# Kernel optimization log

Hardware: AMD Instinct MI355X
Metric: run time of the kernel (lower is better)

## Reference

```python
import jax, jax.numpy as jnp
import numpy as np

I, H, O, K = 64, 512, 3, 6  # input, hidden, output classes, num heads


def setup_inputs() -> dict:
    key = jax.random.key(0)
    ks = jax.random.split(key, 8)
    B, T = 256, 512
    s = 0.05
    return {
        "x": jax.random.normal(ks[0], (B, T, I), dtype=jnp.float32),
        "W_ih": jax.random.normal(ks[1], (4 * H, I), dtype=jnp.float32) * s,
        "W_hh": jax.random.normal(ks[2], (4 * H, H), dtype=jnp.float32) * s,
        "b_ih": jax.random.normal(ks[3], (4 * H,), dtype=jnp.float32) * s,
        "b_hh": jax.random.normal(ks[4], (4 * H,), dtype=jnp.float32) * s,
        "W_heads": jax.random.normal(ks[5], (K, O, H), dtype=jnp.float32) * s,
        "b_heads": jax.random.normal(ks[6], (K, O), dtype=jnp.float32) * s,
    }


def _lstm_last_h(x, W_ih, W_hh, b_ih, b_hh):
    # x: [B, T, I]; returns final hidden state h_T: [B, H]
    B = x.shape[0]
    h0 = jnp.zeros((B, H), dtype=x.dtype)
    c0 = jnp.zeros((B, H), dtype=x.dtype)
    # precompute input projections for all timesteps: [T, B, 4H]
    x_proj = jnp.einsum('bti,gi->tbg', x, W_ih) + b_ih + b_hh

    def step(carry, xp_t):
        h, c = carry
        gates = xp_t + h @ W_hh.T  # [B, 4H]
        i_g, f_g, g_g, o_g = jnp.split(gates, 4, axis=-1)  # PyTorch gate order i,f,g,o
        i_g = jax.nn.sigmoid(i_g)
        f_g = jax.nn.sigmoid(f_g)
        g_g = jnp.tanh(g_g)
        o_g = jax.nn.sigmoid(o_g)
        c = f_g * c + i_g * g_g
        h = o_g * jnp.tanh(c)
        return (h, c), None

    (h_T, _), _ = jax.lax.scan(step, (h0, c0), x_proj)
    return h_T


def reference(x, W_ih, W_hh, b_ih, b_hh, W_heads, b_heads):
    h_T = _lstm_last_h(x, W_ih, W_hh, b_ih, b_hh)  # [B, H]
    # six parallel linear heads on last hidden state -> stacked [6, B, O]
    out = jnp.einsum('koh,bh->kbo', W_heads, h_T) + b_heads[:, None, :]
    return out
```

## Files before the change

### kernel.cpp

```cpp
#include <hip/hip_runtime.h>
#include <hip/hip_bf16.h>
#include <cstdint>

#define TSTEPS 512
#define BATCH  256
#define HID    512
#define INP    64
#define NGRP   16
#define GROWS  16
#define NSL    16
#define NWG    256
#define KTH    16
#define RING   8

typedef __attribute__((ext_vector_type(8))) short short8;
typedef __attribute__((ext_vector_type(4))) float f32x4;
typedef __attribute__((ext_vector_type(2))) float f32x2;
typedef __attribute__((ext_vector_type(2))) unsigned long long ull2;

#define HB_OFF    0
#define HT_OFF    (RING*BATCH*HID*2)
#define FLAGS_OFF (HT_OFF + BATCH*HID*4)
#define FLAGS_SZ  (NGRP*TSTEPS*4)
#define CNT_OFF   (FLAGS_OFF + FLAGS_SZ)
#define ZERO2_SZ  (FLAGS_SZ + 64)

__device__ __forceinline__ unsigned cvtpk(float a, float b) {
    unsigned r;
    asm("v_cvt_pk_bf16_f32 %0, %1, %2" : "=v"(r) : "v"(a), "v"(b));
    return r;
}
__device__ __forceinline__ short8 pack8(float4 a0, float4 a1) {
    uint4 u = { cvtpk(a0.x, a0.y), cvtpk(a0.z, a0.w),
                cvtpk(a1.x, a1.y), cvtpk(a1.z, a1.w) };
    return __builtin_bit_cast(short8, u);
}
__device__ __forceinline__ float sigm(float x)  { return 1.0f/(1.0f + __expf(-x)); }
__device__ __forceinline__ float tanhf_(float x){ return 2.0f/(1.0f + __expf(-2.0f*x)) - 1.0f; }

__global__ void __launch_bounds__(256, 1)
lstm_persist(const float* __restrict__ x,   const float* __restrict__ Wih,
             const float* __restrict__ Whh, const float* __restrict__ bih,
             const float* __restrict__ bhh, const float* __restrict__ Whead,
             const float* __restrict__ bhead, float* __restrict__ out,
             char* __restrict__ ws)
{
    extern __shared__ char lds[];
    const int tid  = threadIdx.x;
    const int lane = tid & 63;
    const int wv   = tid >> 6;
    const int l15  = lane & 15, lq = lane >> 4, l7 = lane & 7;

    unsigned short* hb = (unsigned short*)(ws + HB_OFF);
    float* hT  = (float*)(ws + HT_OFF);
    int* flags = (int*)(ws + FLAGS_OFF);
    int* cnt   = (int*)(ws + CNT_OFF);

    int* org = (int*)(lds + 131056);
    if (tid == 0) {
        unsigned xcd;
        asm volatile("s_getreg_b32 %0, hwreg(HW_REG_XCC_ID)" : "=s"(xcd));
        xcd &= 7u;
        int slot = __hip_atomic_fetch_add(&cnt[xcd], 1, __ATOMIC_RELAXED, __HIP_MEMORY_SCOPE_AGENT) & 31;
        org[0] = (int)xcd * 2 + (slot >> 4);
        org[1] = slot & 15;
    }
    __syncthreads();
    const int g  = org[0];
    const int sl = org[1];
    const int hbase = sl*32 + wv*8;
    const int gsel  = l15 >> 3;

    short8 whh[KTH][2];
    #pragma unroll
    for (int kt = 0; kt < KTH; ++kt)
        #pragma unroll
        for (int nt = 0; nt < 2; ++nt) {
            int grow = (nt*2 + gsel)*HID + hbase + l7;
            const float4* p = (const float4*)(Whh + (size_t)grow*HID + kt*32 + lq*8);
            whh[kt][nt] = pack8(p[0], p[1]);
        }
    short8 wihf[2][2];
    #pragma unroll
    for (int kt = 0; kt < 2; ++kt)
        #pragma unroll
        for (int nt = 0; nt < 2; ++nt) {
            int grow = (nt*2 + gsel)*HID + hbase + l7;
            const float4* p = (const float4*)(Wih + (size_t)grow*INP + kt*32 + lq*8);
            wihf[kt][nt] = pack8(p[0], p[1]);
        }
    float bias0, bias1;
    { int gr = (0*2 + gsel)*HID + hbase + l7; bias0 = bih[gr] + bhh[gr]; }
    { int gr = (1*2 + gsel)*HID + hbase + l7; bias1 = bih[gr] + bhh[gr]; }

    unsigned short* hgrp = hb + (size_t)g*GROWS*HID;
    float*          hTg  = hT + (size_t)g*GROWS*HID;
    int* flg = flags + g*TSTEPS;

    const int skt = tid >> 4, sr = tid & 15;
    char* swp = lds + skt*1024 + sr*16;
    const char* srp = lds + lane*16;

    const float* xrow = x + ((size_t)(g*GROWS + l15)*TSTEPS)*INP + lq*8;

    f32x2 cst = {0.f, 0.f};
    const bool lo = (l15 < 8);

    float4 xv0 = *(const float4*)(xrow);
    float4 xv1 = *(const float4*)(xrow + 4);
    float4 xv2 = *(const float4*)(xrow + 32);
    float4 xv3 = *(const float4*)(xrow + 36);

    #pragma clang loop unroll(disable)
    for (int t = 0; t < TSTEPS; ++t) {
        f32x4 a0 = {bias0, bias0, bias0, bias0};
        f32x4 a1 = {bias1, bias1, bias1, bias1};
        f32x4 b0 = {0.f, 0.f, 0.f, 0.f};
        f32x4 b1 = {0.f, 0.f, 0.f, 0.f};
        {
            short8 af0 = pack8(xv0, xv1);
            short8 af1 = pack8(xv2, xv3);
            a0 = __builtin_amdgcn_mfma_f32_16x16x32_bf16(af0, wihf[0][0], a0, 0, 0, 0);
            a1 = __builtin_amdgcn_mfma_f32_16x16x32_bf16(af0, wihf[0][1], a1, 0, 0, 0);
            b0 = __builtin_amdgcn_mfma_f32_16x16x32_bf16(af1, wihf[1][0], b0, 0, 0, 0);
            b1 = __builtin_amdgcn_mfma_f32_16x16x32_bf16(af1, wihf[1][1], b1, 0, 0, 0);
        }
        __builtin_amdgcn_sched_barrier(0);

        if (t) {
            if (lane == 0) {
                const int* fl = flg + (t-1);
                while (__hip_atomic_load(fl, __ATOMIC_RELAXED, __HIP_MEMORY_SCOPE_AGENT) < NSL) {}
            }
            __builtin_amdgcn_sched_barrier(0);
            asm volatile("" ::: "memory");
        }

        {
            const char* gsrc = (const char*)(hgrp + (size_t)(t & (RING-1))*BATCH*HID)
                               + sr*1024 + skt*64;
            ull2 w0 = *(const ull2*)(gsrc);
            ull2 w1 = *(const ull2*)(gsrc + 16);
            ull2 w2 = *(const ull2*)(gsrc + 32);
            ull2 w3 = *(const ull2*)(gsrc + 48);
            *(ull2*)(swp      ) = w0;
            *(ull2*)(swp + 256) = w1;
            *(ull2*)(swp + 512) = w2;
            *(ull2*)(swp + 768) = w3;
        }
        __syncthreads();

        if (t + 1 < TSTEPS) {
            const float* xn = xrow + (size_t)(t+1)*INP;
            xv0 = *(const float4*)(xn);      xv1 = *(const float4*)(xn + 4);
            xv2 = *(const float4*)(xn + 32); xv3 = *(const float4*)(xn + 36);
        }

        #pragma unroll
        for (int k2 = 0; k2 < 8; ++k2) {
            short8 ae = *(const short8*)(srp + (2*k2  )*1024);
            short8 ao = *(const short8*)(srp + (2*k2+1)*1024);
            a0 = __builtin_amdgcn_mfma_f32_16x16x32_bf16(ae, whh[2*k2  ][0], a0, 0, 0, 0);
            a1 = __builtin_amdgcn_mfma_f32_16x16x32_bf16(ae, whh[2*k2  ][1], a1, 0, 0, 0);
            b0 = __builtin_amdgcn_mfma_f32_16x16x32_bf16(ao, whh[2*k2+1][0], b0, 0, 0, 0);
            b1 = __builtin_amdgcn_mfma_f32_16x16x32_bf16(ao, whh[2*k2+1][1], b1, 0, 0, 0);
        }
        f32x4 acc0 = a0 + b0;
        f32x4 acc1 = a1 + b1;

        float s0[4], s1[4];
        #pragma unroll
        for (int r = 0; r < 4; ++r) {
            s0[r] = __shfl_xor(acc0[r], 8);
            s1[r] = __shfl_xor(acc1[r], 8);
        }
        unsigned short* hbw = hgrp + (size_t)((t+1) & (RING-1))*BATCH*HID;
        #pragma unroll
        for (int rr = 0; rr < 2; ++rr) {
            float iv = lo ? acc0[rr] : s0[rr+2];
            float fv = lo ? s0[rr]   : acc0[rr+2];
            float gv = lo ? acc1[rr] : s1[rr+2];
            float ov = lo ? s1[rr]   : acc1[rr+2];
            float c  = sigm(fv)*cst[rr] + sigm(iv)*tanhf_(gv);
            cst[rr] = c;
            float h  = sigm(ov)*tanhf_(c);
            int row  = lq*4 + rr + (lo ? 0 : 2);
            int idx  = row*HID + hbase + l7;
            hbw[idx] = (unsigned short)(cvtpk(h, h) & 0xffffu);
            if (t == TSTEPS-1) hTg[idx] = h;
        }
        __syncthreads();
        if (tid == 0)
            __hip_atomic_fetch_add(&flg[t], 1, __ATOMIC_RELAXED, __HIP_MEMORY_SCOPE_AGENT);
    }

    if (sl == 0) {
        if (tid == 0) {
            const int* fl = flg + (TSTEPS-1);
            while (__hip_atomic_load(fl, __ATOMIC_RELAXED, __HIP_MEMORY_SCOPE_AGENT) < NSL) {}
        }
        asm volatile("" ::: "memory");
        __syncthreads();
        {
            const float4* gp = (const float4*)((const char*)hTg + tid*128);
            float4* wp = (float4*)(lds + tid*128);
            #pragma unroll
            for (int j = 0; j < 8; ++j) wp[j] = gp[j];
        }
        __syncthreads();
        const float* hsm = (const float*)lds;
        for (int idx = tid; idx < 6*GROWS*3; idx += 256) {
            int k = idx / (GROWS*3), rem = idx % (GROWS*3);
            int row = rem / 3, o = rem % 3;
            const float* wp = Whead + ((size_t)k*3 + o)*HID;
            const float* hp = hsm + row*HID;
            float s = 0.f;
            for (int hh = 0; hh < HID; hh += 4) {
                float4 hv = *(const float4*)(hp + hh);
                float4 wv = *(const float4*)(wp + hh);
                s += hv.x*wv.x + hv.y*wv.y + hv.z*wv.z + hv.w*wv.w;
            }
            out[((size_t)k*BATCH + g*GROWS + row)*3 + o] = s + bhead[k*3 + o];
        }
    }
}

extern "C" void kernel_launch(void* const* d_in, const int* in_sizes, int n_in,
                              void* d_out, int out_size, void* d_ws, size_t ws_size,
                              hipStream_t stream) {
    (void)in_sizes; (void)n_in; (void)out_size; (void)ws_size;
    const float* x     = (const float*)d_in[0];
    const float* Wih   = (const float*)d_in[1];
    const float* Whh   = (const float*)d_in[2];
    const float* bih   = (const float*)d_in[3];
    const float* bhh   = (const float*)d_in[4];
    const float* Whead = (const float*)d_in[5];
    const float* bhead = (const float*)d_in[6];
    char* ws = (char*)d_ws;

    (void)hipFuncSetAttribute((const void*)lstm_persist,
                              hipFuncAttributeMaxDynamicSharedMemorySize, 131072);

    (void)hipMemsetAsync(ws + HB_OFF, 0, BATCH*HID*2, stream);
    (void)hipMemsetAsync(ws + FLAGS_OFF, 0, ZERO2_SZ, stream);

    hipLaunchKernelGGL(lstm_persist, dim3(NWG), dim3(256), 131072, stream,
                       x, Wih, Whh, bih, bhh, Whead, bhead, (float*)d_out, ws);
}
```

Measured before the change: 1.107 ms.

## Use per-slice monotonic flags, direct global-to-LDS loads, and transposed MFMA gate layout

Replaces the per-timestep atomic counter with one monotonic progress flag per slice. Each slice publishes with a store, and each wave polls only the four slices whose h columns it consumes, so the barrier becomes finer-grained with less contention. The h-state staging now uses global_load_lds to copy straight into shared memory with a manual vmcnt wait, instead of loading through registers. The MFMA operands are swapped so each lane holds all four gates of one hidden unit, which removes the cross-lane shuffles before the cell update. This relies on correct per-wave partial synchronization and careful waitcnt ordering, so any mistake there risks races.

```diff
diff --git a/kernel.cpp b/kernel.cpp
--- a/kernel.cpp
+++ b/kernel.cpp
@@ -16,12 +16,11 @@
 typedef __attribute__((ext_vector_type(8))) short short8;
 typedef __attribute__((ext_vector_type(4))) float f32x4;
 typedef __attribute__((ext_vector_type(2))) float f32x2;
-typedef __attribute__((ext_vector_type(2))) unsigned long long ull2;
 
 #define HB_OFF    0
 #define HT_OFF    (RING*BATCH*HID*2)
 #define FLAGS_OFF (HT_OFF + BATCH*HID*4)
-#define FLAGS_SZ  (NGRP*TSTEPS*4)
+#define FLAGS_SZ  (NGRP*NSL*64)
 #define CNT_OFF   (FLAGS_OFF + FLAGS_SZ)
 #define ZERO2_SZ  (FLAGS_SZ + 64)
 
@@ -37,6 +36,12 @@
 }
 __device__ __forceinline__ float sigm(float x)  { return 1.0f/(1.0f + __expf(-x)); }
 __device__ __forceinline__ float tanhf_(float x){ return 2.0f/(1.0f + __expf(-2.0f*x)) - 1.0f; }
+
+__device__ __forceinline__ void gload_lds16(const void* g, void* l) {
+    __builtin_amdgcn_global_load_lds(
+        (const __attribute__((address_space(1))) unsigned*)g,
+        (__attribute__((address_space(3))) unsigned*)l, 16, 0, 0);
+}
 
 __global__ void __launch_bounds__(256, 1)
 lstm_persist(const float* __restrict__ x,   const float* __restrict__ Wih,
@@ -49,11 +54,11 @@
     const int tid  = threadIdx.x;
     const int lane = tid & 63;
     const int wv   = tid >> 6;
-    const int l15  = lane & 15, lq = lane >> 4, l7 = lane & 7;
+    const int l15  = lane & 15, lq = lane >> 4;
 
     unsigned short* hb = (unsigned short*)(ws + HB_OFF);
     float* hT  = (float*)(ws + HT_OFF);
-    int* flags = (int*)(ws + FLAGS_OFF);
+    unsigned* flags = (unsigned*)(ws + FLAGS_OFF);
     int* cnt   = (int*)(ws + CNT_OFF);
 
     int* org = (int*)(lds + 131056);
@@ -68,43 +73,45 @@
     __syncthreads();
     const int g  = org[0];
     const int sl = org[1];
-    const int hbase = sl*32 + wv*8;
-    const int gsel  = l15 >> 3;
+    const int hb8 = sl*32 + wv*8;
 
     short8 whh[KTH][2];
     #pragma unroll
     for (int kt = 0; kt < KTH; ++kt)
         #pragma unroll
-        for (int nt = 0; nt < 2; ++nt) {
-            int grow = (nt*2 + gsel)*HID + hbase + l7;
+        for (int m = 0; m < 2; ++m) {
+            int grow = (l15 & 3)*HID + hb8 + m*4 + (l15 >> 2);
             const float4* p = (const float4*)(Whh + (size_t)grow*HID + kt*32 + lq*8);
-            whh[kt][nt] = pack8(p[0], p[1]);
+            whh[kt][m] = pack8(p[0], p[1]);
         }
     short8 wihf[2][2];
     #pragma unroll
     for (int kt = 0; kt < 2; ++kt)
         #pragma unroll
-        for (int nt = 0; nt < 2; ++nt) {
-            int grow = (nt*2 + gsel)*HID + hbase + l7;
+        for (int m = 0; m < 2; ++m) {
+            int grow = (l15 & 3)*HID + hb8 + m*4 + (l15 >> 2);
             const float4* p = (const float4*)(Wih + (size_t)grow*INP + kt*32 + lq*8);
-            wihf[kt][nt] = pack8(p[0], p[1]);
-        }
-    float bias0, bias1;
-    { int gr = (0*2 + gsel)*HID + hbase + l7; bias0 = bih[gr] + bhh[gr]; }
-    { int gr = (1*2 + gsel)*HID + hbase + l7; bias1 = bih[gr] + bhh[gr]; }
+            wihf[kt][m] = pack8(p[0], p[1]);
+        }
+    f32x4 bias[2];
+    #pragma unroll
+    for (int m = 0; m < 2; ++m)
+        #pragma unroll
+        for (int r = 0; r < 4; ++r) {
+            int hc = hb8 + m*4 + lq;
+            bias[m][r] = bih[r*HID + hc] + bhh[r*HID + hc];
+        }
 
     unsigned short* hgrp = hb + (size_t)g*GROWS*HID;
     float*          hTg  = hT + (size_t)g*GROWS*HID;
-    int* flg = flags + g*TSTEPS;
-
-    const int skt = tid >> 4, sr = tid & 15;
-    char* swp = lds + skt*1024 + sr*16;
-    const char* srp = lds + lane*16;
+
+    unsigned* flg   = flags + (size_t)g*NSL*16;
+    unsigned* fpub  = flg + sl*16;
+    const unsigned* fpoll = flg + (wv*4 + lq)*16;
 
     const float* xrow = x + ((size_t)(g*GROWS + l15)*TSTEPS)*INP + lq*8;
 
     f32x2 cst = {0.f, 0.f};
-    const bool lo = (l15 < 8);
 
     float4 xv0 = *(const float4*)(xrow);
     float4 xv1 = *(const float4*)(xrow + 4);
@@ -113,93 +120,86 @@
 
     #pragma clang loop unroll(disable)
     for (int t = 0; t < TSTEPS; ++t) {
-        f32x4 a0 = {bias0, bias0, bias0, bias0};
-        f32x4 a1 = {bias1, bias1, bias1, bias1};
-        f32x4 b0 = {0.f, 0.f, 0.f, 0.f};
-        f32x4 b1 = {0.f, 0.f, 0.f, 0.f};
-        {
-            short8 af0 = pack8(xv0, xv1);
-            short8 af1 = pack8(xv2, xv3);
-            a0 = __builtin_amdgcn_mfma_f32_16x16x32_bf16(af0, wihf[0][0], a0, 0, 0, 0);
-            a1 = __builtin_amdgcn_mfma_f32_16x16x32_bf16(af0, wihf[0][1], a1, 0, 0, 0);
-            b0 = __builtin_amdgcn_mfma_f32_16x16x32_bf16(af1, wihf[1][0], b0, 0, 0, 0);
-            b1 = __builtin_amdgcn_mfma_f32_16x16x32_bf16(af1, wihf[1][1], b1, 0, 0, 0);
-        }
+        short8 bfx0 = pack8(xv0, xv1);
+        short8 bfx1 = pack8(xv2, xv3);
         __builtin_amdgcn_sched_barrier(0);
 
         if (t) {
-            if (lane == 0) {
-                const int* fl = flg + (t-1);
-                while (__hip_atomic_load(fl, __ATOMIC_RELAXED, __HIP_MEMORY_SCOPE_AGENT) < NSL) {}
+            if (l15 == 0) {
+                while (__hip_atomic_load(fpoll, __ATOMIC_RELAXED, __HIP_MEMORY_SCOPE_AGENT)
+                       < (unsigned)t) {}
             }
             __builtin_amdgcn_sched_barrier(0);
             asm volatile("" ::: "memory");
         }
 
         {
-            const char* gsrc = (const char*)(hgrp + (size_t)(t & (RING-1))*BATCH*HID)
-                               + sr*1024 + skt*64;
-            ull2 w0 = *(const ull2*)(gsrc);
-            ull2 w1 = *(const ull2*)(gsrc + 16);
-            ull2 w2 = *(const ull2*)(gsrc + 32);
-            ull2 w3 = *(const ull2*)(gsrc + 48);
-            *(ull2*)(swp      ) = w0;
-            *(ull2*)(swp + 256) = w1;
-            *(ull2*)(swp + 512) = w2;
-            *(ull2*)(swp + 768) = w3;
-        }
-        __syncthreads();
-
-        if (t + 1 < TSTEPS) {
-            const float* xn = xrow + (size_t)(t+1)*INP;
+            const char* hsrc = (const char*)(hgrp + (size_t)(t & (RING-1))*BATCH*HID)
+                               + l15*1024 + lq*16;
+            #pragma unroll
+            for (int j = 0; j < 4; ++j) {
+                int kt = wv*4 + j;
+                gload_lds16(hsrc + kt*64, lds + kt*1024);
+            }
+        }
+        __builtin_amdgcn_sched_barrier(0);
+        {
+            int tn = (t + 1 < TSTEPS) ? t + 1 : t;
+            const float* xn = xrow + (size_t)tn*INP;
             xv0 = *(const float4*)(xn);      xv1 = *(const float4*)(xn + 4);
             xv2 = *(const float4*)(xn + 32); xv3 = *(const float4*)(xn + 36);
         }
-
+        __builtin_amdgcn_sched_barrier(0);
+        asm volatile("s_waitcnt vmcnt(4)" ::: "memory");
+        __builtin_amdgcn_sched_barrier(0);
+        __builtin_amdgcn_s_barrier();
+        __builtin_amdgcn_sched_barrier(0);
+
+        f32x4 a0 = bias[0], a1 = bias[1];
+        f32x4 b0 = {0.f,0.f,0.f,0.f}, b1 = {0.f,0.f,0.f,0.f};
+        a0 = __builtin_amdgcn_mfma_f32_16x16x32_bf16(wihf[0][0], bfx0, a0, 0, 0, 0);
+        a1 = __builtin_amdgcn_mfma_f32_16x16x32_bf16(wihf[0][1], bfx0, a1, 0, 0, 0);
+        b0 = __builtin_amdgcn_mfma_f32_16x16x32_bf16(wihf[1][0], bfx1, b0, 0, 0, 0);
+        b1 = __builtin_amdgcn_mfma_f32_16x16x32_bf16(wihf[1][1], bfx1, b1, 0, 0, 0);
         #pragma unroll
         for (int k2 = 0; k2 < 8; ++k2) {
-            short8 ae = *(const short8*)(srp + (2*k2  )*1024);
-            short8 ao = *(const short8*)(srp + (2*k2+1)*1024);
-            a0 = __builtin_amdgcn_mfma_f32_16x16x32_bf16(ae, whh[2*k2  ][0], a0, 0, 0, 0);
-            a1 = __builtin_amdgcn_mfma_f32_16x16x32_bf16(ae, whh[2*k2  ][1], a1, 0, 0, 0);
-            b0 = __builtin_amdgcn_mfma_f32_16x16x32_bf16(ao, whh[2*k2+1][0], b0, 0, 0, 0);
-            b1 = __builtin_amdgcn_mfma_f32_16x16x32_bf16(ao, whh[2*k2+1][1], b1, 0, 0, 0);
+            short8 be = *(const short8*)(lds + (2*k2  )*1024 + lane*16);
+            short8 bo = *(const short8*)(lds + (2*k2+1)*1024 + lane*16);
+            a0 = __builtin_amdgcn_mfma_f32_16x16x32_bf16(whh[2*k2  ][0], be, a0, 0, 0, 0);
+            a1 = __builtin_amdgcn_mfma_f32_16x16x32_bf16(whh[2*k2  ][1], be, a1, 0, 0, 0);
+            b0 = __builtin_amdgcn_mfma_f32_16x16x32_bf16(whh[2*k2+1][0], bo, b0, 0, 0, 0);
+            b1 = __builtin_amdgcn_mfma_f32_16x16x32_bf16(whh[2*k2+1][1], bo, b1, 0, 0, 0);
         }
         f32x4 acc0 = a0 + b0;
         f32x4 acc1 = a1 + b1;
 
-        float s0[4], s1[4];
-        #pragma unroll
-        for (int r = 0; r < 4; ++r) {
-            s0[r] = __shfl_xor(acc0[r], 8);
-            s1[r] = __shfl_xor(acc1[r], 8);
-        }
         unsigned short* hbw = hgrp + (size_t)((t+1) & (RING-1))*BATCH*HID;
         #pragma unroll
-        for (int rr = 0; rr < 2; ++rr) {
-            float iv = lo ? acc0[rr] : s0[rr+2];
-            float fv = lo ? s0[rr]   : acc0[rr+2];
-            float gv = lo ? acc1[rr] : s1[rr+2];
-            float ov = lo ? s1[rr]   : acc1[rr+2];
-            float c  = sigm(fv)*cst[rr] + sigm(iv)*tanhf_(gv);
-            cst[rr] = c;
-            float h  = sigm(ov)*tanhf_(c);
-            int row  = lq*4 + rr + (lo ? 0 : 2);
-            int idx  = row*HID + hbase + l7;
+        for (int m = 0; m < 2; ++m) {
+            f32x4 A = m ? acc1 : acc0;
+            float c = sigm(A[1])*cst[m] + sigm(A[0])*tanhf_(A[2]);
+            cst[m] = c;
+            float h = sigm(A[3])*tanhf_(c);
+            int idx = l15*HID + hb8 + m*4 + lq;
             hbw[idx] = (unsigned short)(cvtpk(h, h) & 0xffffu);
             if (t == TSTEPS-1) hTg[idx] = h;
         }
         __syncthreads();
         if (tid == 0)
-            __hip_atomic_fetch_add(&flg[t], 1, __ATOMIC_RELAXED, __HIP_MEMORY_SCOPE_AGENT);
+            __hip_atomic_store(fpub, (unsigned)(t+1),
+                               __ATOMIC_RELAXED, __HIP_MEMORY_SCOPE_AGENT);
     }
 
     if (sl == 0) {
-        if (tid == 0) {
-            const int* fl = flg + (TSTEPS-1);
-            while (__hip_atomic_load(fl, __ATOMIC_RELAXED, __HIP_MEMORY_SCOPE_AGENT) < NSL) {}
-        }
-        asm volatile("" ::: "memory");
+        {
+            unsigned v;
+            do {
+                v = (lane < NSL)
+                    ? __hip_atomic_load(flg + lane*16, __ATOMIC_RELAXED, __HIP_MEMORY_SCOPE_AGENT)
+                    : (unsigned)TSTEPS;
+            } while (!__all(v >= (unsigned)TSTEPS));
+            asm volatile("" ::: "memory");
+        }
         __syncthreads();
         {
             const float4* gp = (const float4*)((const char*)hTg + tid*128);
@@ -217,8 +217,8 @@
             float s = 0.f;
             for (int hh = 0; hh < HID; hh += 4) {
                 float4 hv = *(const float4*)(hp + hh);
-                float4 wv = *(const float4*)(wp + hh);
-                s += hv.x*wv.x + hv.y*wv.y + hv.z*wv.z + hv.w*wv.w;
+                float4 wv2 = *(const float4*)(wp + hh);
+                s += hv.x*wv2.x + hv.y*wv2.y + hv.z*wv2.z + hv.w*wv2.w;
             }
             out[((size_t)k*BATCH + g*GROWS + row)*3 + o] = s + bhead[k*3 + o];
         }
```

Result: slower. 1.284 ms (+16.0%).
